# Kernel tuning notes

Hardware: AMD Instinct MI355X
Metric: run time of the kernel (lower is better)

The kernel has to match this reference:

```python
import jax, jax.numpy as jnp
import numpy as np

N_NODES = 50000
D_FEAT = 128
N_EDGES_1 = 800_000
N_EDGES_2 = 2_400_000


def setup_inputs() -> dict:
    key = jax.random.key(0)
    k = jax.random.split(key, 7)
    x = jax.random.normal(k[0], (N_NODES, D_FEAT), dtype=jnp.float32)
    row1 = jax.random.randint(k[1], (N_EDGES_1,), 0, N_NODES, dtype=jnp.int32)
    col1 = jax.random.randint(k[2], (N_EDGES_1,), 0, N_NODES, dtype=jnp.int32)
    vals1 = jax.random.uniform(k[3], (N_EDGES_1,), dtype=jnp.float32)
    row2 = jax.random.randint(k[4], (N_EDGES_2,), 0, N_NODES, dtype=jnp.int32)
    col2 = jax.random.randint(k[5], (N_EDGES_2,), 0, N_NODES, dtype=jnp.int32)
    vals2 = jax.random.uniform(k[6], (N_EDGES_2,), dtype=jnp.float32)
    return {"x": x, "row1": row1, "col1": col1, "vals1": vals1,
            "row2": row2, "col2": col2, "vals2": vals2}


def _spmm(row, col, vals, x, n_nodes):
    # (A @ x)[i] = sum_{e: row[e]==i} vals[e] * x[col[e]]
    msgs = vals[:, None] * x[col]          # [E, d] gathered, weighted messages
    return jax.ops.segment_sum(msgs, row, num_segments=n_nodes)  # [N, d]


def reference(x, row1, col1, vals1, row2, col2, vals2):
    x1 = _spmm(row1, col1, vals1, x, N_NODES)   # 1-hop aggregation
    x2 = _spmm(row2, col2, vals2, x, N_NODES)   # 2-hop aggregation
    return jnp.concatenate([x1, x2], axis=1)    # [N, 2d]
```

## Files before the change

kernel.cpp:

```cpp
#include <hip/hip_runtime.h>


constexpr int D = 128;
constexpr int OUT_STRIDE = 256;
constexpr int NBMAX = 800;
constexpr int BATCH = 4096;
constexpr int LRECS = 3840;

struct KP {
  const float* x;
  const int* row1; const int* col1; const float* vals1;
  const int* row2; const int* col2; const float* vals2;
  float* out;
  int n, e1, e2, nx4, nb, cap1, cap2, t1, ntasks;
  int* gcur;
  unsigned short* xb;
  uint2* seg1;
  uint2* seg2;
};

__device__ __forceinline__ unsigned short f2b(float f) {
  unsigned u = __float_as_uint(f);
  u += 0x7fffu + ((u >> 16) & 1u);
  return (unsigned short)(u >> 16);
}
__device__ __forceinline__ float blo(unsigned u) { return __uint_as_float(u << 16); }
__device__ __forceinline__ float bhi(unsigned u) { return __uint_as_float(u & 0xffff0000u); }

__launch_bounds__(256)
__global__ void cvt_zero_k(KP p) {
  const int i = blockIdx.x * 256 + threadIdx.x;
  const int GT = gridDim.x * 256;
  for (int j = i; j < 2 * p.nb; j += GT) p.gcur[j] = 0;
  for (int j = i; j < p.nx4; j += GT) {
    const float4 v = ((const float4*)p.x)[j];
    ushort4 o; o.x = f2b(v.x); o.y = f2b(v.y); o.z = f2b(v.z); o.w = f2b(v.w);
    ((ushort4*)p.xb)[j] = o;
  }
}

__launch_bounds__(256)
__global__ void scatter_k(KP p) {
  __shared__ int cnts[NBMAX];
  __shared__ int curs[NBMAX];
  __shared__ int gbase[NBMAX];
  const int tid = threadIdx.x;
  const int nb  = p.nb;

  const int task  = blockIdx.x;
  const int hop   = (task >= p.t1);
  const int tbase = (hop ? (task - p.t1) : task) * BATCH;
  const int E     = hop ? p.e2 : p.e1;
  const int m     = min(BATCH, E - tbase);
  const int* rowp = hop ? p.row2 : p.row1;
  const int* colp = hop ? p.col2 : p.col1;
  const float* vp = hop ? p.vals2 : p.vals1;
  const int cap   = hop ? p.cap2 : p.cap1;
  uint2* seg      = hop ? p.seg2 : p.seg1;
  int* gc         = p.gcur + (hop ? nb : 0);

  for (int b = tid; b < NBMAX; b += 256) { cnts[b] = 0; curs[b] = 0; }
  __syncthreads();

  #pragma unroll
  for (int k = 0; k < BATCH / 1024; ++k) {
    const int i4 = tid + k * 256;
    const int e0 = i4 * 4;
    if (e0 < m) {
      if (e0 + 3 < m) {
        const int4 r = ((const int4*)(rowp + tbase))[i4];
        atomicAdd(&cnts[r.x >> 6], 1);
        atomicAdd(&cnts[r.y >> 6], 1);
        atomicAdd(&cnts[r.z >> 6], 1);
        atomicAdd(&cnts[r.w >> 6], 1);
      } else {
        for (int j = e0; j < m; ++j) atomicAdd(&cnts[rowp[tbase + j] >> 6], 1);
      }
    }
  }
  __syncthreads();

  for (int i = tid; i < nb; i += 256) {
    const int b = (i + task * 37) % nb;
    const int c = cnts[b];
    if (c) gbase[b] = atomicAdd(&gc[b], c);
  }
  __syncthreads();

  #pragma unroll
  for (int k = 0; k < BATCH / 1024; ++k) {
    const int i4 = tid + k * 256;
    const int e0 = i4 * 4;
    if (e0 < m) {
      if (e0 + 3 < m) {
        const int4  rr = ((const int4*)(rowp + tbase))[i4];
        const int4  cc = ((const int4*)(colp + tbase))[i4];
        const float4 vv = ((const float4*)(vp + tbase))[i4];
        {
          const int r = rr.x, b = r >> 6;
          const int pos = gbase[b] + atomicAdd(&curs[b], 1);
          if (pos < cap)
            seg[(size_t)b * cap + pos] =
              make_uint2((unsigned)cc.x | ((unsigned)(r & 63) << 16), __float_as_uint(vv.x));
        }
        {
          const int r = rr.y, b = r >> 6;
          const int pos = gbase[b] + atomicAdd(&curs[b], 1);
          if (pos < cap)
            seg[(size_t)b * cap + pos] =
              make_uint2((unsigned)cc.y | ((unsigned)(r & 63) << 16), __float_as_uint(vv.y));
        }
        {
          const int r = rr.z, b = r >> 6;
          const int pos = gbase[b] + atomicAdd(&curs[b], 1);
          if (pos < cap)
            seg[(size_t)b * cap + pos] =
              make_uint2((unsigned)cc.z | ((unsigned)(r & 63) << 16), __float_as_uint(vv.z));
        }
        {
          const int r = rr.w, b = r >> 6;
          const int pos = gbase[b] + atomicAdd(&curs[b], 1);
          if (pos < cap)
            seg[(size_t)b * cap + pos] =
              make_uint2((unsigned)cc.w | ((unsigned)(r & 63) << 16), __float_as_uint(vv.w));
        }
      } else {
        for (int j = e0; j < m; ++j) {
          const int r = rowp[tbase + j], b = r >> 6;
          const int pos = gbase[b] + atomicAdd(&curs[b], 1);
          if (pos < cap)
            seg[(size_t)b * cap + pos] =
              make_uint2((unsigned)colp[tbase + j] | ((unsigned)(r & 63) << 16),
                         __float_as_uint(vp[tbase + j]));
        }
      }
    }
  }
}

__launch_bounds__(256)
__global__ void sort_gather_k(KP p) {
  __shared__ uint2 lrecs[LRECS];
  __shared__ int rstart[65];
  __shared__ int lcur[64];
  const int tid  = threadIdx.x;
  const int lane = tid & 63;
  const int wid  = tid >> 6;
  const int nb   = p.nb;
  const int hop  = (blockIdx.x < nb) ? 1 : 0;
  const int b    = hop ? blockIdx.x : blockIdx.x - nb;
  const int cap  = hop ? p.cap2 : p.cap1;
  const uint2* seg = (hop ? p.seg2 : p.seg1) + (size_t)b * cap;
  const int cnt  = min(p.gcur[(hop ? nb : 0) + b], cap);
  const uint4* xq = (const uint4*)p.xb;

  if (tid < 64) lcur[tid] = 0;
  __syncthreads();
  for (int t = tid; t < cnt; t += 256)
    atomicAdd(&lcur[(seg[t].x >> 16) & 63u], 1);
  __syncthreads();

  if (tid < 64) {
    const int c = lcur[tid];
    int acc = c;
    #pragma unroll
    for (int d = 1; d < 64; d <<= 1) { int t = __shfl_up(acc, d); if (lane >= d) acc += t; }
    const int ex = acc - c;
    rstart[tid] = ex;
    lcur[tid] = ex;
    if (tid == 63) rstart[64] = acc;
  }
  __syncthreads();

  for (int t = tid; t < cnt; t += 256) {
    const uint2 rec = seg[t];
    const int rl = (int)((rec.x >> 16) & 63u);
    const int pos = atomicAdd(&lcur[rl], 1);
    lrecs[pos] = rec;
  }
  __syncthreads();

  const int g   = lane >> 4;
  const int sub = lane & 15;
  const int rbase = b * 64;

  for (int r = wid; r < 64; r += 4) {
    const int rg = rbase + r;
    if (rg >= p.n) break;
    const int rs = rstart[r];
    const int re = rstart[r + 1];
    float a0 = 0.f, a1 = 0.f, a2 = 0.f, a3 = 0.f;
    float a4 = 0.f, a5 = 0.f, a6 = 0.f, a7 = 0.f;
    if (re > rs) {
      auto LD = [&](int idx, float& v, uint4& xv) {
        const uint2 q = lrecs[idx < re ? idx : re - 1];
        v = (idx < re) ? __uint_as_float(q.y) : 0.f;
        xv = xq[(q.x & 0xffffu) * 16u + (unsigned)sub];
      };
      #define FMA_G(v, xv)                                            \
        a0 = fmaf(v, blo(xv.x), a0); a1 = fmaf(v, bhi(xv.x), a1);     \
        a2 = fmaf(v, blo(xv.y), a2); a3 = fmaf(v, bhi(xv.y), a3);     \
        a4 = fmaf(v, blo(xv.z), a4); a5 = fmaf(v, bhi(xv.z), a5);     \
        a6 = fmaf(v, blo(xv.w), a6); a7 = fmaf(v, bhi(xv.w), a7);

      float v0, v1, v2, v3; uint4 x0, x1, x2, x3;
      const int j0 = rs + g;
      LD(j0, v0, x0); LD(j0 + 4, v1, x1); LD(j0 + 8, v2, x2); LD(j0 + 12, v3, x3);
      const int iters = (re - rs + 15) >> 4;
      for (int it = 1; it < iters; ++it) {
        const int jn = j0 + (it << 4);
        FMA_G(v0, x0); LD(jn,      v0, x0);
        FMA_G(v1, x1); LD(jn + 4,  v1, x1);
        FMA_G(v2, x2); LD(jn + 8,  v2, x2);
        FMA_G(v3, x3); LD(jn + 12, v3, x3);
      }
      FMA_G(v0, x0); FMA_G(v1, x1); FMA_G(v2, x2); FMA_G(v3, x3);
      #undef FMA_G

      a0 += __shfl_xor(a0, 16); a0 += __shfl_xor(a0, 32);
      a1 += __shfl_xor(a1, 16); a1 += __shfl_xor(a1, 32);
      a2 += __shfl_xor(a2, 16); a2 += __shfl_xor(a2, 32);
      a3 += __shfl_xor(a3, 16); a3 += __shfl_xor(a3, 32);
      a4 += __shfl_xor(a4, 16); a4 += __shfl_xor(a4, 32);
      a5 += __shfl_xor(a5, 16); a5 += __shfl_xor(a5, 32);
      a6 += __shfl_xor(a6, 16); a6 += __shfl_xor(a6, 32);
      a7 += __shfl_xor(a7, 16); a7 += __shfl_xor(a7, 32);
    }
    if (g == 0) {
      float* op = p.out + (size_t)rg * OUT_STRIDE + hop * D + sub * 8;
      ((float4*)op)[0] = make_float4(a0, a1, a2, a3);
      ((float4*)op)[1] = make_float4(a4, a5, a6, a7);
    }
  }
}

extern "C" void kernel_launch(void* const* d_in, const int* in_sizes, int n_in,
                              void* d_out, int out_size, void* d_ws, size_t ws_size,
                              hipStream_t stream) {
  KP p;
  p.x     = (const float*)d_in[0];
  p.row1  = (const int*)  d_in[1];
  p.col1  = (const int*)  d_in[2];
  p.vals1 = (const float*)d_in[3];
  p.row2  = (const int*)  d_in[4];
  p.col2  = (const int*)  d_in[5];
  p.vals2 = (const float*)d_in[6];
  p.out   = (float*)d_out;

  p.e1  = in_sizes[1];
  p.e2  = in_sizes[4];
  p.n   = out_size / OUT_STRIDE;
  p.nx4 = in_sizes[0] / 4;
  p.nb  = (p.n + 63) >> 6;
  if (p.nb > NBMAX || p.n > 65535) return;

  {
    const float m1 = (float)p.e1 / p.nb, m2 = (float)p.e2 / p.nb;
    p.cap1 = ((int)(m1 + 10.f * __builtin_sqrtf(m1) + 64.f) + 7) & ~7;
    p.cap2 = ((int)(m2 + 10.f * __builtin_sqrtf(m2) + 64.f) + 7) & ~7;
    if (p.cap1 > LRECS) p.cap1 = LRECS;
    if (p.cap2 > LRECS) p.cap2 = LRECS;
  }
  p.t1     = (p.e1 + BATCH - 1) / BATCH;
  p.ntasks = p.t1 + (p.e2 + BATCH - 1) / BATCH;

  char* w = (char*)d_ws;
  size_t off = 0;
  p.gcur = (int*)w;                       off += (size_t)(2 * p.nb) * 4;
  off = (off + 15) & ~(size_t)15;
  p.xb   = (unsigned short*)(w + off);    off += (size_t)in_sizes[0] * 2;
  off = (off + 15) & ~(size_t)15;
  p.seg1 = (uint2*)(w + off);             off += (size_t)p.nb * p.cap1 * 8;
  p.seg2 = (uint2*)(w + off);             off += (size_t)p.nb * p.cap2 * 8;
  if (ws_size < off) return;

  cvt_zero_k   <<<1024,     256, 0, stream>>>(p);
  scatter_k    <<<p.ntasks, 256, 0, stream>>>(p);
  sort_gather_k<<<2 * p.nb, 256, 0, stream>>>(p);
}
```

Baseline: 304.3 us.

## Stage edges in shared memory for coalesced bucket writes; fuse bf16 conversion

The scatter kernel now loads each edge batch once into registers and builds a bucket-sorted copy in shared memory using a wave-scan prefix sum. It then writes records to the global segment buffers in contiguous runs, replacing the old scattered per-edge stores and removing the second global read of row, col and vals. The fp32-to-bf16 conversion of x moves into the scatter kernel, and a tiny single-block kernel now only zeroes the counters. The costs are a larger shared-memory footprint (32 KB of staging per block), which may limit occupancy, and the bucket id now packed into the upper bits of each record's metadata word.

After: 265.7 us. 12.7% less time.

```diff
diff --git a/kernel.cpp b/kernel.cpp
--- a/kernel.cpp
+++ b/kernel.cpp
@@ -27,25 +27,20 @@
 __device__ __forceinline__ float blo(unsigned u) { return __uint_as_float(u << 16); }
 __device__ __forceinline__ float bhi(unsigned u) { return __uint_as_float(u & 0xffff0000u); }
 
-__launch_bounds__(256)
-__global__ void cvt_zero_k(KP p) {
-  const int i = blockIdx.x * 256 + threadIdx.x;
-  const int GT = gridDim.x * 256;
-  for (int j = i; j < 2 * p.nb; j += GT) p.gcur[j] = 0;
-  for (int j = i; j < p.nx4; j += GT) {
-    const float4 v = ((const float4*)p.x)[j];
-    ushort4 o; o.x = f2b(v.x); o.y = f2b(v.y); o.z = f2b(v.z); o.w = f2b(v.w);
-    ((ushort4*)p.xb)[j] = o;
-  }
-}
-
-__launch_bounds__(256)
+__global__ void zero_k(KP p) {
+  for (int j = threadIdx.x; j < 2 * p.nb; j += 256) p.gcur[j] = 0;
+}
+
+__launch_bounds__(256, 4)
 __global__ void scatter_k(KP p) {
+  __shared__ uint2 srecs[BATCH];
   __shared__ int cnts[NBMAX];
   __shared__ int curs[NBMAX];
-  __shared__ int gbase[NBMAX];
-  const int tid = threadIdx.x;
-  const int nb  = p.nb;
+  __shared__ int wsum[4];
+  const int tid  = threadIdx.x;
+  const int lane = tid & 63;
+  const int wid  = tid >> 6;
+  const int nb   = p.nb;
 
   const int task  = blockIdx.x;
   const int hop   = (task >= p.t1);
@@ -59,82 +54,101 @@
   uint2* seg      = hop ? p.seg2 : p.seg1;
   int* gc         = p.gcur + (hop ? nb : 0);
 
+  {
+    const int per  = (p.nx4 + (int)gridDim.x - 1) / (int)gridDim.x;
+    const int jend = min(p.nx4, (task + 1) * per);
+    for (int j = task * per + tid; j < jend; j += 256) {
+      const float4 v = ((const float4*)p.x)[j];
+      ushort4 o; o.x = f2b(v.x); o.y = f2b(v.y); o.z = f2b(v.z); o.w = f2b(v.w);
+      ((ushort4*)p.xb)[j] = o;
+    }
+  }
+
   for (int b = tid; b < NBMAX; b += 256) { cnts[b] = 0; curs[b] = 0; }
-  __syncthreads();
-
-  #pragma unroll
-  for (int k = 0; k < BATCH / 1024; ++k) {
-    const int i4 = tid + k * 256;
-    const int e0 = i4 * 4;
-    if (e0 < m) {
-      if (e0 + 3 < m) {
-        const int4 r = ((const int4*)(rowp + tbase))[i4];
-        atomicAdd(&cnts[r.x >> 6], 1);
-        atomicAdd(&cnts[r.y >> 6], 1);
-        atomicAdd(&cnts[r.z >> 6], 1);
-        atomicAdd(&cnts[r.w >> 6], 1);
-      } else {
-        for (int j = e0; j < m; ++j) atomicAdd(&cnts[rowp[tbase + j] >> 6], 1);
+
+  int   rowv[16]; int colv[16]; float valv[16];
+  #pragma unroll
+  for (int k = 0; k < 4; ++k) {
+    const int i4 = tid + (k << 8);
+    const int e0 = i4 << 2;
+    if (e0 + 3 < m) {
+      const int4  r = ((const int4*)(rowp + tbase))[i4];
+      const int4  c = ((const int4*)(colp + tbase))[i4];
+      const float4 v = ((const float4*)(vp + tbase))[i4];
+      rowv[k*4+0] = r.x; rowv[k*4+1] = r.y; rowv[k*4+2] = r.z; rowv[k*4+3] = r.w;
+      colv[k*4+0] = c.x; colv[k*4+1] = c.y; colv[k*4+2] = c.z; colv[k*4+3] = c.w;
+      valv[k*4+0] = v.x; valv[k*4+1] = v.y; valv[k*4+2] = v.z; valv[k*4+3] = v.w;
+    } else {
+      #pragma unroll
+      for (int c2 = 0; c2 < 4; ++c2) {
+        const int e = e0 + c2;
+        if (e < m) {
+          rowv[k*4+c2] = rowp[tbase + e];
+          colv[k*4+c2] = colp[tbase + e];
+          valv[k*4+c2] = vp[tbase + e];
+        } else {
+          rowv[k*4+c2] = -1; colv[k*4+c2] = 0; valv[k*4+c2] = 0.f;
+        }
       }
     }
+  }
+  __syncthreads();
+
+  #pragma unroll
+  for (int i = 0; i < 16; ++i)
+    if (rowv[i] >= 0) atomicAdd(&cnts[rowv[i] >> 6], 1);
+  __syncthreads();
+
+  int c0 = 0, c1 = 0, c2 = 0, c3 = 0, s = 0;
+  const int b0 = tid * 4;
+  if (b0 < NBMAX) {
+    c0 = cnts[b0]; c1 = cnts[b0 + 1]; c2 = cnts[b0 + 2]; c3 = cnts[b0 + 3];
+    s = c0 + c1 + c2 + c3;
+  }
+  int acc = s;
+  #pragma unroll
+  for (int d = 1; d < 64; d <<= 1) { int t = __shfl_up(acc, d); if (lane >= d) acc += t; }
+  if (lane == 63) wsum[wid] = acc;
+  __syncthreads();
+  int woff = 0;
+  #pragma unroll
+  for (int w = 0; w < 4; ++w) if (w < wid) woff += wsum[w];
+  if (b0 < NBMAX) {
+    const int ex = woff + acc - s;
+    curs[b0]     = ex;
+    curs[b0 + 1] = ex + c0;
+    curs[b0 + 2] = ex + c0 + c1;
+    curs[b0 + 3] = ex + c0 + c1 + c2;
   }
   __syncthreads();
 
   for (int i = tid; i < nb; i += 256) {
     const int b = (i + task * 37) % nb;
     const int c = cnts[b];
-    if (c) gbase[b] = atomicAdd(&gc[b], c);
-  }
-  __syncthreads();
-
-  #pragma unroll
-  for (int k = 0; k < BATCH / 1024; ++k) {
-    const int i4 = tid + k * 256;
-    const int e0 = i4 * 4;
-    if (e0 < m) {
-      if (e0 + 3 < m) {
-        const int4  rr = ((const int4*)(rowp + tbase))[i4];
-        const int4  cc = ((const int4*)(colp + tbase))[i4];
-        const float4 vv = ((const float4*)(vp + tbase))[i4];
-        {
-          const int r = rr.x, b = r >> 6;
-          const int pos = gbase[b] + atomicAdd(&curs[b], 1);
-          if (pos < cap)
-            seg[(size_t)b * cap + pos] =
-              make_uint2((unsigned)cc.x | ((unsigned)(r & 63) << 16), __float_as_uint(vv.x));
-        }
-        {
-          const int r = rr.y, b = r >> 6;
-          const int pos = gbase[b] + atomicAdd(&curs[b], 1);
-          if (pos < cap)
-            seg[(size_t)b * cap + pos] =
-              make_uint2((unsigned)cc.y | ((unsigned)(r & 63) << 16), __float_as_uint(vv.y));
-        }
-        {
-          const int r = rr.z, b = r >> 6;
-          const int pos = gbase[b] + atomicAdd(&curs[b], 1);
-          if (pos < cap)
-            seg[(size_t)b * cap + pos] =
-              make_uint2((unsigned)cc.z | ((unsigned)(r & 63) << 16), __float_as_uint(vv.z));
-        }
-        {
-          const int r = rr.w, b = r >> 6;
-          const int pos = gbase[b] + atomicAdd(&curs[b], 1);
-          if (pos < cap)
-            seg[(size_t)b * cap + pos] =
-              make_uint2((unsigned)cc.w | ((unsigned)(r & 63) << 16), __float_as_uint(vv.w));
-        }
-      } else {
-        for (int j = e0; j < m; ++j) {
-          const int r = rowp[tbase + j], b = r >> 6;
-          const int pos = gbase[b] + atomicAdd(&curs[b], 1);
-          if (pos < cap)
-            seg[(size_t)b * cap + pos] =
-              make_uint2((unsigned)colp[tbase + j] | ((unsigned)(r & 63) << 16),
-                         __float_as_uint(vp[tbase + j]));
-        }
-      }
-    }
+    if (c) {
+      const int g = atomicAdd(&gc[b], c);
+      cnts[b] = g - curs[b];
+    }
+  }
+  __syncthreads();
+
+  #pragma unroll
+  for (int i = 0; i < 16; ++i) {
+    const int r = rowv[i];
+    if (r >= 0) {
+      const int b = r >> 6;
+      const int pos = atomicAdd(&curs[b], 1);
+      const unsigned meta = (unsigned)colv[i] | ((unsigned)(r & 63) << 16) | ((unsigned)b << 22);
+      srecs[pos] = make_uint2(meta, __float_as_uint(valv[i]));
+    }
+  }
+  __syncthreads();
+
+  for (int t = tid; t < m; t += 256) {
+    const uint2 rec = srecs[t];
+    const int b = rec.x >> 22;
+    const int pos = t + cnts[b];
+    if (pos < cap) seg[(size_t)b * cap + pos] = rec;
   }
 }
 
@@ -274,7 +288,7 @@
   p.seg2 = (uint2*)(w + off);             off += (size_t)p.nb * p.cap2 * 8;
   if (ws_size < off) return;
 
-  cvt_zero_k   <<<1024,     256, 0, stream>>>(p);
+  zero_k       <<<1,        256, 0, stream>>>(p);
   scatter_k    <<<p.ntasks, 256, 0, stream>>>(p);
   sort_gather_k<<<2 * p.nb, 256, 0, stream>>>(p);
 }
```
